# Optimization experiments

Hardware: AMD Instinct MI355X
Metric: run time of the kernel (lower is better)

Reference implementation:

```python
import jax, jax.numpy as jnp
import numpy as np

D_MODEL = 2048
N_HEADS = 16
HEAD_DIM = D_MODEL // N_HEADS


def setup_inputs() -> dict:
    key = jax.random.key(0)
    ks = jax.random.split(key, 6)
    B, T = 4, 2048
    scale = 1.0 / np.sqrt(D_MODEL)
    x = jax.random.normal(ks[0], (B, T, D_MODEL), dtype=jnp.float32)
    wq = jax.random.normal(ks[1], (D_MODEL, D_MODEL), dtype=jnp.float32) * scale
    wk = jax.random.normal(ks[2], (D_MODEL, D_MODEL), dtype=jnp.float32) * scale
    wv = jax.random.normal(ks[3], (D_MODEL, D_MODEL), dtype=jnp.float32) * scale
    wo = jax.random.normal(ks[4], (D_MODEL, D_MODEL), dtype=jnp.float32) * scale
    bo = jnp.zeros((D_MODEL,), dtype=jnp.float32)
    return {"x": x, "wq": wq, "wk": wk, "wv": wv, "wo": wo, "bo": bo}


def reference(x, wq, wk, wv, wo, bo):
    B, T, C = x.shape
    H, Dh = N_HEADS, HEAD_DIM
    # torch nn.Linear: y = x @ W.T
    q = (x @ wq.T).reshape(B, T, H, Dh).transpose(0, 2, 1, 3)  # (B,H,T,Dh)
    k = (x @ wk.T).reshape(B, T, H, Dh).transpose(0, 2, 1, 3)
    v = (x @ wv.T).reshape(B, T, H, Dh).transpose(0, 2, 1, 3)
    scores = jnp.einsum('bhqd,bhkd->bhqk', q, k) / np.sqrt(Dh).astype(np.float32)
    attn = jax.nn.softmax(scores, axis=-1)  # no causal mask in source
    out = jnp.einsum('bhqk,bhkd->bhqd', attn, v)
    out = out.transpose(0, 2, 1, 3).reshape(B, T, C)
    return out @ wo.T + bo
```

## Files before the change

kernel.cpp:

```cpp
#include <hip/hip_runtime.h>
#include <hip/hip_bf16.h>
#include <math.h>

typedef __attribute__((ext_vector_type(8))) __bf16 bf16x8;
typedef __attribute__((ext_vector_type(4))) float floatx4;

__device__ inline unsigned short f2u(float f) {
  __hip_bfloat16 h = __float2bfloat16(f);
  unsigned short u;
  __builtin_memcpy(&u, &h, 2);
  return u;
}

__device__ inline floatx4 mfma16(bf16x8 a, bf16x8 b, floatx4 c) {
  return __builtin_amdgcn_mfma_f32_16x16x32_bf16(a, b, c, 0, 0, 0);
}

__device__ inline void gload_lds16(const unsigned short* g, unsigned short* l) {
  __builtin_amdgcn_global_load_lds(
      (__attribute__((address_space(1))) void*)g,
      (__attribute__((address_space(3))) void*)l,
      16, 0, 0);
}

__global__ __launch_bounds__(256) void castk(const float* __restrict__ in,
                                             unsigned short* __restrict__ out,
                                             int n4, float scale) {
  int i = blockIdx.x * 256 + threadIdx.x;
  if (i >= n4) return;
  const float4 v = reinterpret_cast<const float4*>(in)[i];
  ushort4 o;
  o.x = f2u(v.x * scale);
  o.y = f2u(v.y * scale);
  o.z = f2u(v.z * scale);
  o.w = f2u(v.w * scale);
  reinterpret_cast<ushort4*>(out)[i] = o;
}

template <int OUT>
__global__ __launch_bounds__(512, 2)
void gemm256(const unsigned short* __restrict__ A,
             const unsigned short* __restrict__ B,
             unsigned short* __restrict__ Cb,
             float* __restrict__ Cf,
             const float* __restrict__ bias,
             int M, int N, int K) {
  extern __shared__ unsigned short lds[];
  const int t = threadIdx.x;
  const int w = t >> 6;
  const int l = t & 63;
  const int wm = w >> 2;
  const int wn = w & 3;
  const int fr = l & 15;
  const int fkb = l >> 4;
  const int key = fr & 7;
  const int sslot = (l & 7) ^ (l >> 3);

  const int m0 = blockIdx.y * 256;
  const int n0 = blockIdx.x * 256;
  const int T = K >> 6;

  auto stage = [&](const unsigned short* G, int rb, int kt2, int h, int ldsbase) {
    const int d2 = kt2 & 1;
    const int rt = h * 128 + w * 16 + (l >> 3);
    const unsigned short* s0 = G + (size_t)(rb + rt) * K + kt2 * 64 + sslot * 8;
    unsigned short* dst = lds + ldsbase + d2 * 16384 + h * 8192 + w * 1024;
    gload_lds16(s0, dst);
    gload_lds16(s0 + (size_t)8 * K, dst + 512);
  };

  floatx4 acc[8][4];
#pragma unroll
  for (int m = 0; m < 8; m++)
#pragma unroll
    for (int n = 0; n < 4; n++) acc[m][n] = (floatx4){0.f, 0.f, 0.f, 0.f};

  stage(A, m0, 0, 0, 0);
  stage(A, m0, 0, 1, 0);
  stage(B, n0, 0, 0, 32768);
  stage(B, n0, 0, 1, 32768);
  if (1 < T) {
    stage(B, n0, 1, 0, 32768);
    stage(B, n0, 1, 1, 32768);
    asm volatile("s_waitcnt vmcnt(4)" ::: "memory");
  } else {
    asm volatile("s_waitcnt vmcnt(0)" ::: "memory");
  }
  __builtin_amdgcn_s_barrier();

#define GPHASE(q, STAGE_STMT)                                               \
  {                                                                         \
    bf16x8 a00 = *reinterpret_cast<const bf16x8*>(                          \
        Ab + (wm * 128 + (2 * (q)) * 16 + fr) * 64 + ((fkb ^ key)) * 8);    \
    bf16x8 a01 = *reinterpret_cast<const bf16x8*>(                          \
        Ab + (wm * 128 + (2 * (q)) * 16 + fr) * 64 + (((4 + fkb) ^ key)) * 8); \
    bf16x8 a10 = *reinterpret_cast<const bf16x8*>(                          \
        Ab + (wm * 128 + (2 * (q) + 1) * 16 + fr) * 64 + ((fkb ^ key)) * 8);\
    bf16x8 a11 = *reinterpret_cast<const bf16x8*>(                          \
        Ab + (wm * 128 + (2 * (q) + 1) * 16 + fr) * 64 + (((4 + fkb) ^ key)) * 8); \
    STAGE_STMT;                                                             \
    __builtin_amdgcn_s_barrier();                                           \
    asm volatile("s_waitcnt lgkmcnt(0)");                                   \
    __builtin_amdgcn_s_setprio(1);                                          \
    _Pragma("unroll")                                                       \
    for (int n = 0; n < 4; n++) {                                           \
      acc[2 * (q)][n] = mfma16(a00, bfr[0][n], acc[2 * (q)][n]);            \
      acc[2 * (q)][n] = mfma16(a01, bfr[1][n], acc[2 * (q)][n]);            \
      acc[2 * (q) + 1][n] = mfma16(a10, bfr[0][n], acc[2 * (q) + 1][n]);    \
      acc[2 * (q) + 1][n] = mfma16(a11, bfr[1][n], acc[2 * (q) + 1][n]);    \
    }                                                                       \
    __builtin_amdgcn_s_setprio(0);                                          \
    __builtin_amdgcn_s_barrier();                                           \
  }

  for (int kt = 0; kt < T; ++kt) {
    const int d = kt & 1;
    const unsigned short* Ab = lds + d * 16384;
    const unsigned short* Bb = lds + 32768 + d * 16384;

    bf16x8 bfr[2][4];
#pragma unroll
    for (int kk = 0; kk < 2; kk++)
#pragma unroll
      for (int n = 0; n < 4; n++)
        bfr[kk][n] = *reinterpret_cast<const bf16x8*>(
            Bb + (wn * 64 + n * 16 + fr) * 64 + (((kk * 4 + fkb) ^ key)) * 8);

    GPHASE(0, if (kt + 1 < T) stage(A, m0, kt + 1, 0, 0));
    GPHASE(1, if (kt + 1 < T) stage(A, m0, kt + 1, 1, 0));
    GPHASE(2, if (kt + 2 < T) stage(B, n0, kt + 2, 0, 32768));
    GPHASE(3, {
      if (kt + 2 < T) {
        stage(B, n0, kt + 2, 1, 32768);
        asm volatile("s_waitcnt vmcnt(4)" ::: "memory");
      } else {
        asm volatile("s_waitcnt vmcnt(0)" ::: "memory");
      }
    });
  }
#undef GPHASE

  const int er = (l >> 4) * 4;
  const int ec = l & 15;
#pragma unroll
  for (int m = 0; m < 8; m++) {
#pragma unroll
    for (int n = 0; n < 4; n++) {
      const int col = n0 + wn * 64 + n * 16 + ec;
      if (OUT == 2) {
        const int hv = col >> 7, dh = col & 127;
        const int row0 = m0 + wm * 128 + m * 16 + er;
        const int bb = row0 >> 11;
        const int t0 = row0 & 2047;
        unsigned short* vp =
            Cb + (((size_t)(bb * 16 + hv)) * 128 + dh) * 2048 + t0;
#pragma unroll
        for (int r = 0; r < 4; r++) vp[r] = f2u(acc[m][n][r]);
      } else {
#pragma unroll
        for (int r = 0; r < 4; r++) {
          const int row = m0 + wm * 128 + m * 16 + er + r;
          if (OUT == 1) {
            Cf[(size_t)row * N + col] = acc[m][n][r] + bias[col];
          } else {
            Cb[(size_t)row * N + col] = f2u(acc[m][n][r]);
          }
        }
      }
    }
  }
}

__global__ __launch_bounds__(256, 2)
void attn_kernel(const unsigned short* __restrict__ Y2,
                 const unsigned short* __restrict__ Vtg,
                 unsigned short* __restrict__ att) {
  __shared__ unsigned short Kt[2][64 * 128];
  __shared__ unsigned short Vt[128 * 64];
  __shared__ unsigned short Pl[4][32 * 72];

  const int t = threadIdx.x;
  const int w = t >> 6;
  const int l = t & 63;
  const int bid = blockIdx.x;
  const int bh = bid & 63;
  const int qt = bid >> 6;
  const int b = bh >> 4;
  const int h = bh & 15;

  const size_t ybase = (size_t)b * 2048 * 4096 + (size_t)h * 128;
  const unsigned short* Qp = Y2 + ybase;
  const unsigned short* Kp = Y2 + ybase + 2048;
  const unsigned short* Vp = Vtg + (size_t)bh * 128 * 2048;

  const int fr = l & 15;
  const int fkb = l >> 4;
  const int key = fr & 7;

  const int ksr = t >> 4;
  const int ksl = (t & 15) ^ (ksr & 7);
  const unsigned short* Ksrc = Kp + (size_t)ksr * 4096 + ksl * 8;

  const int vsr = t >> 3;
  const int vsl = (t & 7) ^ (vsr & 7);
  const unsigned short* Vsrc = Vp + (size_t)vsr * 2048 + vsl * 8;

  bf16x8 qf[2][4];
#pragma unroll
  for (int i = 0; i < 2; i++)
#pragma unroll
    for (int kk = 0; kk < 4; kk++)
      qf[i][kk] = *reinterpret_cast<const bf16x8*>(
          &Qp[(size_t)(qt * 128 + w * 32 + i * 16 + fr) * 4096 + kk * 32 + fkb * 8]);

  floatx4 oacc[2][8];
#pragma unroll
  for (int i = 0; i < 2; i++)
#pragma unroll
    for (int nt = 0; nt < 8; nt++) oacc[i][nt] = (floatx4){0.f, 0.f, 0.f, 0.f};
  float mrun[2][4], lrun[2][4];
#pragma unroll
  for (int i = 0; i < 2; i++)
#pragma unroll
    for (int r = 0; r < 4; r++) {
      mrun[i][r] = -INFINITY;
      lrun[i][r] = 0.f;
    }

  unsigned short* Pw = &Pl[w][0];

#pragma unroll
  for (int c = 0; c < 4; c++)
    gload_lds16(Ksrc + (size_t)c * 16 * 4096, &Kt[0][c * 2048 + w * 512]);
  __syncthreads();

  int cur = 0;
  for (int kv = 0; kv < 2048; kv += 64) {
#pragma unroll
    for (int c = 0; c < 4; c++)
      gload_lds16(Vsrc + (size_t)c * 32 * 2048 + kv, &Vt[c * 2048 + w * 512]);

    floatx4 sacc[2][4];
#pragma unroll
    for (int i = 0; i < 2; i++)
#pragma unroll
      for (int nt = 0; nt < 4; nt++) sacc[i][nt] = (floatx4){0.f, 0.f, 0.f, 0.f};
#pragma unroll
    for (int nt = 0; nt < 4; nt++) {
#pragma unroll
      for (int kk = 0; kk < 4; kk++) {
        bf16x8 kf = *reinterpret_cast<const bf16x8*>(
            &Kt[cur][((nt * 16 + fr) * 16 + ((kk * 4 + fkb) ^ key)) * 8]);
        sacc[0][nt] = mfma16(qf[0][kk], kf, sacc[0][nt]);
        sacc[1][nt] = mfma16(qf[1][kk], kf, sacc[1][nt]);
      }
    }

#pragma unroll
    for (int i = 0; i < 2; i++) {
#pragma unroll
      for (int r = 0; r < 4; r++) {
        float s0 = sacc[i][0][r], s1 = sacc[i][1][r];
        float s2 = sacc[i][2][r], s3 = sacc[i][3][r];
        float mx = fmaxf(fmaxf(s0, s1), fmaxf(s2, s3));
        mx = fmaxf(mx, __shfl_xor(mx, 1));
        mx = fmaxf(mx, __shfl_xor(mx, 2));
        mx = fmaxf(mx, __shfl_xor(mx, 4));
        mx = fmaxf(mx, __shfl_xor(mx, 8));
        if (mx > mrun[i][r] + 8.0f) {
          float alpha = __expf(mrun[i][r] - mx);
          mrun[i][r] = mx;
          lrun[i][r] *= alpha;
#pragma unroll
          for (int nt = 0; nt < 8; nt++) oacc[i][nt][r] *= alpha;
        }
        const float m = mrun[i][r];
        float p0 = __expf(s0 - m);
        float p1 = __expf(s1 - m);
        float p2 = __expf(s2 - m);
        float p3 = __expf(s3 - m);
        float ps = (p0 + p1) + (p2 + p3);
        ps += __shfl_xor(ps, 1);
        ps += __shfl_xor(ps, 2);
        ps += __shfl_xor(ps, 4);
        ps += __shfl_xor(ps, 8);
        lrun[i][r] += ps;
        const int pr = i * 16 + fkb * 4 + r;
        Pw[pr * 72 + fr] = f2u(p0);
        Pw[pr * 72 + 16 + fr] = f2u(p1);
        Pw[pr * 72 + 32 + fr] = f2u(p2);
        Pw[pr * 72 + 48 + fr] = f2u(p3);
      }
    }

    __syncthreads();

    if (kv + 64 < 2048) {
#pragma unroll
      for (int c = 0; c < 4; c++)
        gload_lds16(Ksrc + (size_t)(kv + 64 + c * 16) * 4096,
                    &Kt[cur ^ 1][c * 2048 + w * 512]);
    }

    bf16x8 pf[2][2];
#pragma unroll
    for (int i = 0; i < 2; i++) {
      pf[i][0] = *reinterpret_cast<const bf16x8*>(&Pw[(i * 16 + fr) * 72 + fkb * 8]);
      pf[i][1] = *reinterpret_cast<const bf16x8*>(&Pw[(i * 16 + fr) * 72 + 32 + fkb * 8]);
    }
#pragma unroll
    for (int nt = 0; nt < 8; nt++) {
      const unsigned short* vr = &Vt[(nt * 16 + fr) * 64];
      bf16x8 vf0 = *reinterpret_cast<const bf16x8*>(vr + (fkb ^ key) * 8);
      bf16x8 vf1 = *reinterpret_cast<const bf16x8*>(vr + ((fkb + 4) ^ key) * 8);
#pragma unroll
      for (int i = 0; i < 2; i++) {
        oacc[i][nt] = mfma16(pf[i][0], vf0, oacc[i][nt]);
        oacc[i][nt] = mfma16(pf[i][1], vf1, oacc[i][nt]);
      }
    }

    __syncthreads();
    cur ^= 1;
  }

#pragma unroll
  for (int i = 0; i < 2; i++) {
#pragma unroll
    for (int r = 0; r < 4; r++) {
      const float inv = 1.0f / lrun[i][r];
      const int row = qt * 128 + w * 32 + i * 16 + fkb * 4 + r;
      unsigned short* op = att + ((size_t)b * 2048 + row) * 2048 + h * 128 + fr;
#pragma unroll
      for (int nt = 0; nt < 8; nt++) op[nt * 16] = f2u(oacc[i][nt][r] * inv);
    }
  }
}

extern "C" void kernel_launch(void* const* d_in, const int* in_sizes, int n_in,
                              void* d_out, int out_size, void* d_ws, size_t ws_size,
                              hipStream_t stream) {
  const float* x = (const float*)d_in[0];
  const float* wq = (const float*)d_in[1];
  const float* wk = (const float*)d_in[2];
  const float* wv = (const float*)d_in[3];
  const float* wo = (const float*)d_in[4];
  const float* bo = (const float*)d_in[5];

  unsigned short* ws = (unsigned short*)d_ws;
  unsigned short* x16 = ws;
  unsigned short* wqkv16 = x16 + 16777216;
  unsigned short* wo16 = wqkv16 + 12582912;
  unsigned short* Y2 = wo16 + 4194304;
  unsigned short* Vtg = Y2 + 33554432;
  unsigned short* att16 = Vtg + 16777216;

  const float sscale = 0.08838834764831845f;

  hipFuncSetAttribute(reinterpret_cast<const void*>(gemm256<0>),
                      hipFuncAttributeMaxDynamicSharedMemorySize, 131072);
  hipFuncSetAttribute(reinterpret_cast<const void*>(gemm256<1>),
                      hipFuncAttributeMaxDynamicSharedMemorySize, 131072);
  hipFuncSetAttribute(reinterpret_cast<const void*>(gemm256<2>),
                      hipFuncAttributeMaxDynamicSharedMemorySize, 131072);

  castk<<<16384, 256, 0, stream>>>(x, x16, 4194304, 1.0f);
  castk<<<4096, 256, 0, stream>>>(wq, wqkv16, 1048576, sscale);
  castk<<<4096, 256, 0, stream>>>(wk, wqkv16 + 4194304, 1048576, 1.0f);
  castk<<<4096, 256, 0, stream>>>(wv, wqkv16 + 8388608, 1048576, 1.0f);
  castk<<<4096, 256, 0, stream>>>(wo, wo16, 1048576, 1.0f);

  dim3 gqk(16, 32);
  gemm256<0><<<gqk, 512, 131072, stream>>>(x16, wqkv16, Y2, nullptr, nullptr,
                                           8192, 4096, 2048);
  dim3 gv(8, 32);
  gemm256<2><<<gv, 512, 131072, stream>>>(x16, wqkv16 + 8388608, Vtg, nullptr,
                                          nullptr, 8192, 2048, 2048);

  attn_kernel<<<1024, 256, 0, stream>>>(Y2, Vtg, att16);

  dim3 go(8, 32);
  gemm256<1><<<go, 512, 131072, stream>>>(att16, wo16, nullptr, (float*)d_out,
                                          bo, 8192, 2048, 2048);
}
```

Baseline: 556.8 us.

## Merge weight casts into one launch and restructure attention K/V LDS prefetch

Replaces four separate weight-cast launches with a single kernel that selects the source and destination tensor from the block index, removing three launch overheads. In the attention kernel, the K tile drops from double to single buffering. The V load for the next tile is now issued after the second barrier, so it overlaps the next score computation instead of being issued at the start of each iteration. This halves K's LDS footprint, which may allow more blocks per CU, but the next K tile is loaded into the same buffer while the current iteration is still running.

Result: faster. 542.0 us (-2.7%).

```diff
diff --git a/kernel.cpp b/kernel.cpp
--- a/kernel.cpp
+++ b/kernel.cpp
@@ -34,6 +34,29 @@
   o.y = f2u(v.y * scale);
   o.z = f2u(v.z * scale);
   o.w = f2u(v.w * scale);
+  reinterpret_cast<ushort4*>(out)[i] = o;
+}
+
+__global__ __launch_bounds__(256) void castw4(const float* __restrict__ wq,
+                                              const float* __restrict__ wk,
+                                              const float* __restrict__ wv,
+                                              const float* __restrict__ wo,
+                                              unsigned short* __restrict__ oq,
+                                              unsigned short* __restrict__ ok,
+                                              unsigned short* __restrict__ ov,
+                                              unsigned short* __restrict__ oo,
+                                              float qscale) {
+  const int tensor = blockIdx.x >> 12;
+  const int i = (blockIdx.x & 4095) * 256 + threadIdx.x;
+  const float* in = tensor == 0 ? wq : tensor == 1 ? wk : tensor == 2 ? wv : wo;
+  unsigned short* out = tensor == 0 ? oq : tensor == 1 ? ok : tensor == 2 ? ov : oo;
+  const float s = tensor == 0 ? qscale : 1.0f;
+  const float4 v = reinterpret_cast<const float4*>(in)[i];
+  ushort4 o;
+  o.x = f2u(v.x * s);
+  o.y = f2u(v.y * s);
+  o.z = f2u(v.z * s);
+  o.w = f2u(v.w * s);
   reinterpret_cast<ushort4*>(out)[i] = o;
 }
 
@@ -175,7 +198,7 @@
 void attn_kernel(const unsigned short* __restrict__ Y2,
                  const unsigned short* __restrict__ Vtg,
                  unsigned short* __restrict__ att) {
-  __shared__ unsigned short Kt[2][64 * 128];
+  __shared__ unsigned short Kt[64 * 128];
   __shared__ unsigned short Vt[128 * 64];
   __shared__ unsigned short Pl[4][32 * 72];
 
@@ -231,15 +254,13 @@
 
 #pragma unroll
   for (int c = 0; c < 4; c++)
-    gload_lds16(Ksrc + (size_t)c * 16 * 4096, &Kt[0][c * 2048 + w * 512]);
+    gload_lds16(Ksrc + (size_t)c * 16 * 4096, &Kt[c * 2048 + w * 512]);
+#pragma unroll
+  for (int c = 0; c < 4; c++)
+    gload_lds16(Vsrc + (size_t)c * 32 * 2048, &Vt[c * 2048 + w * 512]);
   __syncthreads();
 
-  int cur = 0;
   for (int kv = 0; kv < 2048; kv += 64) {
-#pragma unroll
-    for (int c = 0; c < 4; c++)
-      gload_lds16(Vsrc + (size_t)c * 32 * 2048 + kv, &Vt[c * 2048 + w * 512]);
-
     floatx4 sacc[2][4];
 #pragma unroll
     for (int i = 0; i < 2; i++)
@@ -250,7 +271,7 @@
 #pragma unroll
       for (int kk = 0; kk < 4; kk++) {
         bf16x8 kf = *reinterpret_cast<const bf16x8*>(
-            &Kt[cur][((nt * 16 + fr) * 16 + ((kk * 4 + fkb) ^ key)) * 8]);
+            &Kt[((nt * 16 + fr) * 16 + ((kk * 4 + fkb) ^ key)) * 8]);
         sacc[0][nt] = mfma16(qf[0][kk], kf, sacc[0][nt]);
         sacc[1][nt] = mfma16(qf[1][kk], kf, sacc[1][nt]);
       }
@@ -299,7 +320,7 @@
 #pragma unroll
       for (int c = 0; c < 4; c++)
         gload_lds16(Ksrc + (size_t)(kv + 64 + c * 16) * 4096,
-                    &Kt[cur ^ 1][c * 2048 + w * 512]);
+                    &Kt[c * 2048 + w * 512]);
     }
 
     bf16x8 pf[2][2];
@@ -321,7 +342,13 @@
     }
 
     __syncthreads();
-    cur ^= 1;
+
+    if (kv + 64 < 2048) {
+#pragma unroll
+      for (int c = 0; c < 4; c++)
+        gload_lds16(Vsrc + (size_t)c * 32 * 2048 + (kv + 64),
+                    &Vt[c * 2048 + w * 512]);
+    }
   }
 
 #pragma unroll
@@ -365,10 +392,9 @@
                       hipFuncAttributeMaxDynamicSharedMemorySize, 131072);
 
   castk<<<16384, 256, 0, stream>>>(x, x16, 4194304, 1.0f);
-  castk<<<4096, 256, 0, stream>>>(wq, wqkv16, 1048576, sscale);
-  castk<<<4096, 256, 0, stream>>>(wk, wqkv16 + 4194304, 1048576, 1.0f);
-  castk<<<4096, 256, 0, stream>>>(wv, wqkv16 + 8388608, 1048576, 1.0f);
-  castk<<<4096, 256, 0, stream>>>(wo, wo16, 1048576, 1.0f);
+  castw4<<<16384, 256, 0, stream>>>(wq, wk, wv, wo,
+                                    wqkv16, wqkv16 + 4194304,
+                                    wqkv16 + 8388608, wo16, sscale);
 
   dim3 gqk(16, 32);
   gemm256<0><<<gqk, 512, 131072, stream>>>(x16, wqkv16, Y2, nullptr, nullptr,
```
